# Optimization experiments

Hardware: AMD Instinct MI355X
Metric: run time of the kernel (lower is better)

The kernel has to match this reference:

```python
import jax, jax.numpy as jnp
import numpy as np
import math

BS, N, D_MODEL, H = 8, 1024, 512, 8
D_K = D_MODEL // H


def setup_inputs() -> dict:
    key = jax.random.key(0)
    ks = jax.random.split(key, 12)
    s = 1.0 / math.sqrt(D_MODEL)
    inp = {
        "query": jax.random.normal(ks[0], (BS, N, D_MODEL), jnp.float32),
        "key": jax.random.normal(ks[1], (BS, N, D_MODEL), jnp.float32),
        "value": jax.random.normal(ks[2], (BS, N, D_MODEL), jnp.float32),
        "wc_matrix": jax.random.normal(ks[3], (BS, N, N), jnp.float32),
        "Wq": jax.random.normal(ks[4], (D_MODEL, D_MODEL), jnp.float32) * s,
        "bq": jnp.zeros((D_MODEL,), jnp.float32),
        "Wk": jax.random.normal(ks[5], (D_MODEL, D_MODEL), jnp.float32) * s,
        "bk": jnp.zeros((D_MODEL,), jnp.float32),
        "Wv": jax.random.normal(ks[6], (D_MODEL, D_MODEL), jnp.float32) * s,
        "bv": jnp.zeros((D_MODEL,), jnp.float32),
        "Wo": jax.random.normal(ks[7], (D_MODEL, D_MODEL), jnp.float32) * s,
        "bo": jnp.zeros((D_MODEL,), jnp.float32),
    }
    return inp


def _split_heads(x):
    # (bs, N, d_model) -> (bs, h, N, d_k)
    b, n, _ = x.shape
    return x.reshape(b, n, H, D_K).transpose(0, 2, 1, 3)


def reference(query, key, value, wc_matrix, Wq, bq, Wk, bk, Wv, bv, Wo, bo):
    # Linear projections (torch Linear: x @ W.T + b), split into heads
    q = _split_heads(query @ Wq.T + bq)
    k = _split_heads(key @ Wk.T + bk)
    v = _split_heads(value @ Wv.T + bv)

    # scores: (bs, h, N, N)
    scores = jnp.einsum("bhnd,bhmd->bhnm", q, k) / jnp.sqrt(jnp.float32(D_K))
    # WC modulation: scores * softmax(wc)[:, None] + scores  (softmax_wc=True, residual=True)
    wc_sm = jax.nn.softmax(wc_matrix, axis=-1)[:, None]  # (bs, 1, N, N)
    scores = scores * wc_sm + scores
    p_attn = jax.nn.softmax(scores, axis=-1)  # dropout is identity in eval

    a = jnp.einsum("bhnm,bhmd->bhnd", p_attn, v)
    a = a.transpose(0, 2, 1, 3).reshape(query.shape[0], -1, D_MODEL)
    return a @ Wo.T + bo
```

## Files before the change

### kernel.cpp

```cpp
#include <hip/hip_runtime.h>
#include <math.h>


#define BS 8
#define SEQ 1024
#define DM 512
#define NH 8
#define DK 64
#define ROWS (BS * SEQ)

typedef __bf16 bf16_t;
typedef bf16_t bf16x8 __attribute__((ext_vector_type(8)));
typedef bf16_t bf16x4 __attribute__((ext_vector_type(4)));
typedef float f32x4 __attribute__((ext_vector_type(4)));

__device__ inline f32x4 mfma32(bf16x8 a, bf16x8 b, f32x4 c) {
  return __builtin_amdgcn_mfma_f32_16x16x32_bf16(a, b, c, 0, 0, 0);
}

__device__ inline void gload_lds16(const bf16_t* g, bf16_t* l) {
  __builtin_amdgcn_global_load_lds(
      (const __attribute__((address_space(1))) void*)g,
      (__attribute__((address_space(3))) void*)l, 16, 0, 0);
}

__global__ __launch_bounds__(256) void cvt_kernel(
    const float* q, const float* k, const float* v,
    const float* wq, const float* wk, const float* wv, const float* wo,
    bf16_t* xq, bf16_t* xk, bf16_t* xv,
    bf16_t* wqb, bf16_t* wkb, bf16_t* wvb, bf16_t* wob) {
  const float* srcs[7] = {q, k, v, wq, wk, wv, wo};
  bf16_t* dsts[7] = {xq, xk, xv, wqb, wkb, wvb, wob};
  int b = blockIdx.x;
  int seg, boff;
  if (b < 1536) { seg = b >> 9; boff = b & 511; }
  else { seg = 3 + ((b - 1536) >> 5); boff = (b - 1536) & 31; }
  const float* src = srcs[seg] + (size_t)boff * 8192;
  bf16_t* dst = dsts[seg] + (size_t)boff * 8192;
  int t = threadIdx.x;
#pragma unroll
  for (int f = 0; f < 8; ++f) {
    int idx = (f * 256 + t) * 4;
    float4 x = *(const float4*)(src + idx);
    bf16x4 o;
    o[0] = (bf16_t)x.x; o[1] = (bf16_t)x.y; o[2] = (bf16_t)x.z; o[3] = (bf16_t)x.w;
    *(bf16x4*)(dst + idx) = o;
  }
}

__global__ __launch_bounds__(256) void wc_softmax_kernel(const float* __restrict__ wc,
                                                         bf16_t* __restrict__ G) {
  int row = blockIdx.x;
  const float* x = wc + (size_t)row * SEQ;
  bf16_t* y = G + (size_t)row * SEQ;
  int t = threadIdx.x;
  float4 v = *(const float4*)(x + t * 4);
  float m = fmaxf(fmaxf(v.x, v.y), fmaxf(v.z, v.w));
#pragma unroll
  for (int off = 32; off > 0; off >>= 1) m = fmaxf(m, __shfl_xor(m, off, 64));
  __shared__ float sm[4], ss[4];
  int w = t >> 6;
  if ((t & 63) == 0) sm[w] = m;
  __syncthreads();
  m = fmaxf(fmaxf(sm[0], sm[1]), fmaxf(sm[2], sm[3]));
  float4 e;
  e.x = __expf(v.x - m); e.y = __expf(v.y - m);
  e.z = __expf(v.z - m); e.w = __expf(v.w - m);
  float s = e.x + e.y + e.z + e.w;
#pragma unroll
  for (int off = 32; off > 0; off >>= 1) s += __shfl_xor(s, off, 64);
  if ((t & 63) == 0) ss[w] = s;
  __syncthreads();
  s = ss[0] + ss[1] + ss[2] + ss[3];
  float inv = 1.0f / s;
  bf16x4 g;
  g[0] = (bf16_t)(1.0f + e.x * inv);
  g[1] = (bf16_t)(1.0f + e.y * inv);
  g[2] = (bf16_t)(1.0f + e.z * inv);
  g[3] = (bf16_t)(1.0f + e.w * inv);
  *(bf16x4*)(y + t * 4) = g;
}

template <int BM, bool OUTF32>
__device__ inline void gemm_core(const bf16_t* X, const bf16_t* W,
                                 const float* bias, void* Cv,
                                 int mblk, int nblk) {
  __shared__ bf16_t As[2][BM * 32];
  __shared__ bf16_t Bs[2][128 * 32];
  int t = threadIdx.x, lane = t & 63, w = t >> 6;
  int quad = lane >> 4, l15 = lane & 15;
  constexpr int MT = BM / 32;
  int m0w = (w & 1) * (BM / 2), n0w = (w >> 1) * 64;
  int mbase = mblk * BM, nbase = nblk * 128;
  int lr = lane >> 2, l4 = lane & 3;
  f32x4 acc[MT][4] = {};

#pragma unroll
  for (int f = 0; f < BM / 64; ++f) {
    int i = f * 4 + w;
    gload_lds16(X + (size_t)(mbase + i * 16 + lr) * DM + l4 * 8, &As[0][i * 512]);
  }
#pragma unroll
  for (int f = 0; f < 2; ++f) {
    int i = f * 4 + w;
    gload_lds16(W + (size_t)(nbase + i * 16 + lr) * DM + l4 * 8, &Bs[0][i * 512]);
  }

  for (int it = 0; it < 16; ++it) {
    __syncthreads();
    int cb = it & 1;
    if (it + 1 < 16) {
      int kb = (it + 1) * 32, nb = (it + 1) & 1;
#pragma unroll
      for (int f = 0; f < BM / 64; ++f) {
        int i = f * 4 + w;
        gload_lds16(X + (size_t)(mbase + i * 16 + lr) * DM + kb + l4 * 8, &As[nb][i * 512]);
      }
#pragma unroll
      for (int f = 0; f < 2; ++f) {
        int i = f * 4 + w;
        gload_lds16(W + (size_t)(nbase + i * 16 + lr) * DM + kb + l4 * 8, &Bs[nb][i * 512]);
      }
    }
    bf16x8 af[MT], bfr[4];
#pragma unroll
    for (int mt = 0; mt < MT; ++mt)
      af[mt] = *(const bf16x8*)&As[cb][(m0w + mt * 16 + l15) * 32 + quad * 8];
#pragma unroll
    for (int nt = 0; nt < 4; ++nt)
      bfr[nt] = *(const bf16x8*)&Bs[cb][(n0w + nt * 16 + l15) * 32 + quad * 8];
#pragma unroll
    for (int mt = 0; mt < MT; ++mt)
#pragma unroll
      for (int nt = 0; nt < 4; ++nt)
        acc[mt][nt] = mfma32(af[mt], bfr[nt], acc[mt][nt]);
  }

#pragma unroll
  for (int nt = 0; nt < 4; ++nt) {
    int col = nbase + n0w + nt * 16 + l15;
    float bc = bias[col];
#pragma unroll
    for (int mt = 0; mt < MT; ++mt)
#pragma unroll
      for (int r = 0; r < 4; ++r) {
        int row = mbase + m0w + mt * 16 + quad * 4 + r;
        float vv = acc[mt][nt][r] + bc;
        if (OUTF32)
          ((float*)Cv)[(size_t)row * DM + col] = vv;
        else
          ((bf16_t*)Cv)[(size_t)row * DM + col] = (bf16_t)vv;
      }
  }
}

__global__ __launch_bounds__(256) void gemm_qkv_kernel(
    const bf16_t* xq, const bf16_t* xk, const bf16_t* xv,
    const bf16_t* wq, const bf16_t* wk, const bf16_t* wv,
    const float* bq, const float* bk, const float* bv,
    bf16_t* cq, bf16_t* ck, bf16_t* cv) {
  const bf16_t* Xarr[3] = {xq, xk, xv};
  const bf16_t* Warr[3] = {wq, wk, wv};
  const float* barr[3] = {bq, bk, bv};
  bf16_t* Carr[3] = {cq, ck, cv};
  int z = blockIdx.z;
  gemm_core<128, false>(Xarr[z], Warr[z], barr[z], Carr[z], blockIdx.x, blockIdx.y);
}

__global__ __launch_bounds__(256) void gemm_wo_kernel(const bf16_t* X, const bf16_t* W,
                                                      const float* bias, float* C) {
  gemm_core<64, true>(X, W, bias, C, blockIdx.x, blockIdx.y);
}

__global__ __launch_bounds__(256) void vtrans_kernel(const bf16_t* __restrict__ Vb,
                                                     bf16_t* __restrict__ Vt) {
  int mt = blockIdx.x;
  int bh = blockIdx.y;
  int b = bh >> 3, h = bh & 7;
  __shared__ bf16_t Ts[64][66];
  int t = threadIdx.x;
#pragma unroll
  for (int f = 0; f < 2; ++f) {
    int chunk = t + f * 256;
    int row = chunk >> 3;
    int c8 = (chunk & 7) * 8;
    bf16x8 v = *(const bf16x8*)&Vb[(size_t)(b * SEQ + mt * 64 + row) * DM + h * DK + c8];
#pragma unroll
    for (int j = 0; j < 8; ++j) Ts[c8 + j][row] = v[j];
  }
  __syncthreads();
#pragma unroll
  for (int f = 0; f < 2; ++f) {
    int chunk = t + f * 256;
    int d = chunk >> 3;
    int m8 = (chunk & 7) * 8;
    bf16x8 o;
#pragma unroll
    for (int j = 0; j < 8; ++j) o[j] = Ts[d][m8 + j];
    *(bf16x8*)&Vt[((size_t)(bh * DK + d)) * SEQ + mt * 64 + m8] = o;
  }
}

__global__ __launch_bounds__(256) void flash_mfma_kernel(const bf16_t* __restrict__ Qb,
                                                         const bf16_t* __restrict__ Kb,
                                                         const bf16_t* __restrict__ Vt,
                                                         const bf16_t* __restrict__ G,
                                                         bf16_t* __restrict__ Ab) {
  int qt = blockIdx.x, h = blockIdx.y, b = blockIdx.z;
  __shared__ bf16_t Qs[64][72];
  __shared__ bf16_t Ks[64][72];
  __shared__ bf16_t Vs[64][72];
  __shared__ bf16_t Ps[64][72];
  int t = threadIdx.x, lane = t & 63, w = t >> 6;
  int quad = lane >> 4, l15 = lane & 15;

#pragma unroll
  for (int f = 0; f < 2; ++f) {
    int chunk = t + f * 256;
    int row = chunk >> 3, k8 = (chunk & 7) * 8;
    *(bf16x8*)&Qs[row][k8] =
        *(const bf16x8*)&Qb[(size_t)(b * SEQ + qt * 64 + row) * DM + h * DK + k8];
  }
  __syncthreads();
  bf16x8 aq0 = *(const bf16x8*)&Qs[w * 16 + l15][quad * 8];
  bf16x8 aq1 = *(const bf16x8*)&Qs[w * 16 + l15][32 + quad * 8];

  float m_st = -INFINITY, l_st = 0.f;
  f32x4 o[4] = {};
  const size_t grow = (size_t)(b * SEQ + qt * 64 + w * 16 + l15) * SEQ;

  int srow[2], sk8[2];
#pragma unroll
  for (int f = 0; f < 2; ++f) {
    int chunk = t + f * 256;
    srow[f] = chunk >> 3;
    sk8[f] = (chunk & 7) * 8;
  }
  const bf16_t* Kbase = Kb + (size_t)b * SEQ * DM + h * DK;
  const bf16_t* Vbase = Vt + (size_t)(b * NH + h) * DK * SEQ;
  bf16x8 kreg[2], vreg[2];
  bf16x4 greg[4];
#pragma unroll
  for (int f = 0; f < 2; ++f) {
    kreg[f] = *(const bf16x8*)&Kbase[(size_t)srow[f] * DM + sk8[f]];
    vreg[f] = *(const bf16x8*)&Vbase[(size_t)srow[f] * SEQ + sk8[f]];
  }
#pragma unroll
  for (int ct = 0; ct < 4; ++ct)
    greg[ct] = *(const bf16x4*)&G[grow + ct * 16 + quad * 4];

  for (int mt = 0; mt < 16; ++mt) {
    __syncthreads();
#pragma unroll
    for (int f = 0; f < 2; ++f) {
      *(bf16x8*)&Ks[srow[f]][sk8[f]] = kreg[f];
      *(bf16x8*)&Vs[srow[f]][sk8[f]] = vreg[f];
    }
    __syncthreads();
    if (mt + 1 < 16) {
#pragma unroll
      for (int f = 0; f < 2; ++f) {
        kreg[f] = *(const bf16x8*)&Kbase[(size_t)((mt + 1) * 64 + srow[f]) * DM + sk8[f]];
        vreg[f] = *(const bf16x8*)&Vbase[(size_t)srow[f] * SEQ + (mt + 1) * 64 + sk8[f]];
      }
    }

    f32x4 s[4];
#pragma unroll
    for (int ct = 0; ct < 4; ++ct) {
      bf16x8 ak0 = *(const bf16x8*)&Ks[ct * 16 + l15][quad * 8];
      bf16x8 ak1 = *(const bf16x8*)&Ks[ct * 16 + l15][32 + quad * 8];
      f32x4 z = {};
      s[ct] = mfma32(ak1, aq1, mfma32(ak0, aq0, z));
    }

    float sv[4][4];
    float rm = -INFINITY;
#pragma unroll
    for (int ct = 0; ct < 4; ++ct) {
#pragma unroll
      for (int r = 0; r < 4; ++r) {
        float x = s[ct][r] * 0.125f * (float)greg[ct][r];
        sv[ct][r] = x;
        rm = fmaxf(rm, x);
      }
    }
    if (mt + 1 < 16) {
#pragma unroll
      for (int ct = 0; ct < 4; ++ct)
        greg[ct] = *(const bf16x4*)&G[grow + (mt + 1) * 64 + ct * 16 + quad * 4];
    }
    rm = fmaxf(rm, __shfl_xor(rm, 16, 64));
    rm = fmaxf(rm, __shfl_xor(rm, 32, 64));
    float mnew = fmaxf(m_st, rm);
    float alpha = __expf(m_st - mnew);
    m_st = mnew;

    float rs = 0.f;
#pragma unroll
    for (int ct = 0; ct < 4; ++ct) {
      bf16x4 pb;
#pragma unroll
      for (int r = 0; r < 4; ++r) {
        float p = __expf(sv[ct][r] - mnew);
        pb[r] = (bf16_t)p;
        rs += p;
      }
      *(bf16x4*)&Ps[w * 16 + l15][ct * 16 + quad * 4] = pb;
    }
    rs += __shfl_xor(rs, 16, 64);
    rs += __shfl_xor(rs, 32, 64);
    l_st = l_st * alpha + rs;

#pragma unroll
    for (int dt = 0; dt < 4; ++dt) {
      o[dt][0] *= alpha; o[dt][1] *= alpha; o[dt][2] *= alpha; o[dt][3] *= alpha;
    }
#pragma unroll
    for (int c = 0; c < 2; ++c) {
      bf16x8 bp = *(const bf16x8*)&Ps[w * 16 + l15][c * 32 + quad * 8];
#pragma unroll
      for (int dt = 0; dt < 4; ++dt) {
        bf16x8 av = *(const bf16x8*)&Vs[dt * 16 + l15][c * 32 + quad * 8];
        o[dt] = mfma32(av, bp, o[dt]);
      }
    }
  }

  float linv = 1.0f / l_st;
  size_t qrow = (size_t)(b * SEQ + qt * 64 + w * 16 + l15);
#pragma unroll
  for (int dt = 0; dt < 4; ++dt)
#pragma unroll
    for (int r = 0; r < 4; ++r)
      Ab[qrow * DM + h * DK + dt * 16 + quad * 4 + r] = (bf16_t)(o[dt][r] * linv);
}

extern "C" void kernel_launch(void* const* d_in, const int* in_sizes, int n_in,
                              void* d_out, int out_size, void* d_ws, size_t ws_size,
                              hipStream_t stream) {
  const float* query = (const float*)d_in[0];
  const float* key = (const float*)d_in[1];
  const float* value = (const float*)d_in[2];
  const float* wc = (const float*)d_in[3];
  const float* Wq = (const float*)d_in[4];
  const float* bq = (const float*)d_in[5];
  const float* Wk = (const float*)d_in[6];
  const float* bk = (const float*)d_in[7];
  const float* Wv = (const float*)d_in[8];
  const float* bv = (const float*)d_in[9];
  const float* Wo = (const float*)d_in[10];
  const float* bo = (const float*)d_in[11];
  float* out = (float*)d_out;

  const size_t ACT = (size_t)ROWS * DM;
  const size_t WSZ = (size_t)DM * DM;
  bf16_t* Qb = (bf16_t*)d_ws;
  bf16_t* Kb = Qb + ACT;
  bf16_t* Vb = Kb + ACT;
  bf16_t* Vt = Vb + ACT;
  bf16_t* Ab = Vt + ACT;
  bf16_t* G = Ab + ACT;
  bf16_t* Xq = G + (size_t)BS * SEQ * SEQ;
  bf16_t* Xk = Xq + ACT;
  bf16_t* Xv = Xk + ACT;
  bf16_t* Wqb = Xv + ACT;
  bf16_t* Wkb = Wqb + WSZ;
  bf16_t* Wvb = Wkb + WSZ;
  bf16_t* Wob = Wvb + WSZ;

  cvt_kernel<<<1664, 256, 0, stream>>>(query, key, value, Wq, Wk, Wv, Wo,
                                       Xq, Xk, Xv, Wqb, Wkb, Wvb, Wob);

  wc_softmax_kernel<<<BS * SEQ, 256, 0, stream>>>(wc, G);

  gemm_qkv_kernel<<<dim3(ROWS / 128, DM / 128, 3), 256, 0, stream>>>(
      Xq, Xk, Xv, Wqb, Wkb, Wvb, bq, bk, bv, Qb, Kb, Vb);

  vtrans_kernel<<<dim3(16, 64), 256, 0, stream>>>(Vb, Vt);

  flash_mfma_kernel<<<dim3(SEQ / 64, NH, BS), 256, 0, stream>>>(Qb, Kb, Vt, G, Ab);

  gemm_wo_kernel<<<dim3(ROWS / 64, DM / 128), 256, 0, stream>>>(Ab, Wob, bo, out);
}
```

Measured before the change: 230.0 us.

## Fuse prep kernels, write V transposed from GEMM, double-buffer 128-row flash tiles

Merges the fp32-to-bf16 conversion and the wc softmax into one prep launch, with one wave per softmax row instead of one block. The V projection epilogue now writes the per-head transposed layout directly, so the separate transpose kernel and its buffer go away. The flash kernel handles 128 query rows per block (two 16-row subtiles per wave) and double-buffers K/V in LDS, which reuses each K/V tile across more queries and drops one barrier per iteration. In exchange it uses more LDS and registers, and launches half as many flash blocks (512), which may lower occupancy.

```diff
diff --git a/kernel.cpp b/kernel.cpp
--- a/kernel.cpp
+++ b/kernel.cpp
@@ -24,67 +24,72 @@
       (__attribute__((address_space(3))) void*)l, 16, 0, 0);
 }
 
-__global__ __launch_bounds__(256) void cvt_kernel(
+__global__ __launch_bounds__(256) void prep_kernel(
     const float* q, const float* k, const float* v,
     const float* wq, const float* wk, const float* wv, const float* wo,
+    const float* wc,
     bf16_t* xq, bf16_t* xk, bf16_t* xv,
-    bf16_t* wqb, bf16_t* wkb, bf16_t* wvb, bf16_t* wob) {
-  const float* srcs[7] = {q, k, v, wq, wk, wv, wo};
-  bf16_t* dsts[7] = {xq, xk, xv, wqb, wkb, wvb, wob};
-  int b = blockIdx.x;
-  int seg, boff;
-  if (b < 1536) { seg = b >> 9; boff = b & 511; }
-  else { seg = 3 + ((b - 1536) >> 5); boff = (b - 1536) & 31; }
-  const float* src = srcs[seg] + (size_t)boff * 8192;
-  bf16_t* dst = dsts[seg] + (size_t)boff * 8192;
+    bf16_t* wqb, bf16_t* wkb, bf16_t* wvb, bf16_t* wob,
+    bf16_t* G) {
+  int blk = blockIdx.x;
   int t = threadIdx.x;
-#pragma unroll
-  for (int f = 0; f < 8; ++f) {
-    int idx = (f * 256 + t) * 4;
-    float4 x = *(const float4*)(src + idx);
-    bf16x4 o;
-    o[0] = (bf16_t)x.x; o[1] = (bf16_t)x.y; o[2] = (bf16_t)x.z; o[3] = (bf16_t)x.w;
-    *(bf16x4*)(dst + idx) = o;
-  }
-}
-
-__global__ __launch_bounds__(256) void wc_softmax_kernel(const float* __restrict__ wc,
-                                                         bf16_t* __restrict__ G) {
-  int row = blockIdx.x;
-  const float* x = wc + (size_t)row * SEQ;
-  bf16_t* y = G + (size_t)row * SEQ;
-  int t = threadIdx.x;
-  float4 v = *(const float4*)(x + t * 4);
-  float m = fmaxf(fmaxf(v.x, v.y), fmaxf(v.z, v.w));
-#pragma unroll
-  for (int off = 32; off > 0; off >>= 1) m = fmaxf(m, __shfl_xor(m, off, 64));
-  __shared__ float sm[4], ss[4];
-  int w = t >> 6;
-  if ((t & 63) == 0) sm[w] = m;
-  __syncthreads();
-  m = fmaxf(fmaxf(sm[0], sm[1]), fmaxf(sm[2], sm[3]));
-  float4 e;
-  e.x = __expf(v.x - m); e.y = __expf(v.y - m);
-  e.z = __expf(v.z - m); e.w = __expf(v.w - m);
-  float s = e.x + e.y + e.z + e.w;
-#pragma unroll
-  for (int off = 32; off > 0; off >>= 1) s += __shfl_xor(s, off, 64);
-  if ((t & 63) == 0) ss[w] = s;
-  __syncthreads();
-  s = ss[0] + ss[1] + ss[2] + ss[3];
-  float inv = 1.0f / s;
-  bf16x4 g;
-  g[0] = (bf16_t)(1.0f + e.x * inv);
-  g[1] = (bf16_t)(1.0f + e.y * inv);
-  g[2] = (bf16_t)(1.0f + e.z * inv);
-  g[3] = (bf16_t)(1.0f + e.w * inv);
-  *(bf16x4*)(y + t * 4) = g;
+  if (blk < 1664) {
+    const float* srcs[7] = {q, k, v, wq, wk, wv, wo};
+    bf16_t* dsts[7] = {xq, xk, xv, wqb, wkb, wvb, wob};
+    int seg, boff;
+    if (blk < 1536) { seg = blk >> 9; boff = blk & 511; }
+    else { seg = 3 + ((blk - 1536) >> 5); boff = (blk - 1536) & 31; }
+    const float* src = srcs[seg] + (size_t)boff * 8192;
+    bf16_t* dst = dsts[seg] + (size_t)boff * 8192;
+#pragma unroll
+    for (int f = 0; f < 8; ++f) {
+      int idx = (f * 256 + t) * 4;
+      float4 x = *(const float4*)(src + idx);
+      bf16x4 o;
+      o[0] = (bf16_t)x.x; o[1] = (bf16_t)x.y; o[2] = (bf16_t)x.z; o[3] = (bf16_t)x.w;
+      *(bf16x4*)(dst + idx) = o;
+    }
+  } else {
+    int row = (blk - 1664) * 4 + (t >> 6);
+    int l = t & 63;
+    const float* x = wc + (size_t)row * SEQ;
+    bf16_t* y = G + (size_t)row * SEQ;
+    float4 vv[4];
+#pragma unroll
+    for (int j = 0; j < 4; ++j) vv[j] = *(const float4*)(x + l * 4 + j * 256);
+    float m = -INFINITY;
+#pragma unroll
+    for (int j = 0; j < 4; ++j)
+      m = fmaxf(m, fmaxf(fmaxf(vv[j].x, vv[j].y), fmaxf(vv[j].z, vv[j].w)));
+#pragma unroll
+    for (int off = 1; off < 64; off <<= 1) m = fmaxf(m, __shfl_xor(m, off, 64));
+    float4 e[4];
+    float s = 0.f;
+#pragma unroll
+    for (int j = 0; j < 4; ++j) {
+      e[j].x = __expf(vv[j].x - m); e[j].y = __expf(vv[j].y - m);
+      e[j].z = __expf(vv[j].z - m); e[j].w = __expf(vv[j].w - m);
+      s += e[j].x + e[j].y + e[j].z + e[j].w;
+    }
+#pragma unroll
+    for (int off = 1; off < 64; off <<= 1) s += __shfl_xor(s, off, 64);
+    float inv = 1.0f / s;
+#pragma unroll
+    for (int j = 0; j < 4; ++j) {
+      bf16x4 g;
+      g[0] = (bf16_t)(1.0f + e[j].x * inv);
+      g[1] = (bf16_t)(1.0f + e[j].y * inv);
+      g[2] = (bf16_t)(1.0f + e[j].z * inv);
+      g[3] = (bf16_t)(1.0f + e[j].w * inv);
+      *(bf16x4*)(y + l * 4 + j * 256) = g;
+    }
+  }
 }
 
 template <int BM, bool OUTF32>
 __device__ inline void gemm_core(const bf16_t* X, const bf16_t* W,
                                  const float* bias, void* Cv,
-                                 int mblk, int nblk) {
+                                 int mblk, int nblk, bool vt_out) {
   __shared__ bf16_t As[2][BM * 32];
   __shared__ bf16_t Bs[2][128 * 32];
   int t = threadIdx.x, lane = t & 63, w = t >> 6;
@@ -136,21 +141,38 @@
         acc[mt][nt] = mfma32(af[mt], bfr[nt], acc[mt][nt]);
   }
 
-#pragma unroll
-  for (int nt = 0; nt < 4; ++nt) {
-    int col = nbase + n0w + nt * 16 + l15;
-    float bc = bias[col];
-#pragma unroll
-    for (int mt = 0; mt < MT; ++mt)
-#pragma unroll
-      for (int r = 0; r < 4; ++r) {
-        int row = mbase + m0w + mt * 16 + quad * 4 + r;
-        float vv = acc[mt][nt][r] + bc;
-        if (OUTF32)
-          ((float*)Cv)[(size_t)row * DM + col] = vv;
-        else
-          ((bf16_t*)Cv)[(size_t)row * DM + col] = (bf16_t)vv;
-      }
+  if (vt_out) {
+#pragma unroll
+    for (int nt = 0; nt < 4; ++nt) {
+      int col = nbase + n0w + nt * 16 + l15;
+      float bc = bias[col];
+#pragma unroll
+      for (int mt = 0; mt < MT; ++mt) {
+        int row = mbase + m0w + mt * 16 + quad * 4;
+        int bb = row >> 10, ml = row & 1023;
+        bf16x4 vv;
+#pragma unroll
+        for (int r = 0; r < 4; ++r) vv[r] = (bf16_t)(acc[mt][nt][r] + bc);
+        *(bf16x4*)&((bf16_t*)Cv)[((size_t)((bb * NH + (col >> 6)) * DK + (col & 63))) * SEQ + ml] = vv;
+      }
+    }
+  } else {
+#pragma unroll
+    for (int nt = 0; nt < 4; ++nt) {
+      int col = nbase + n0w + nt * 16 + l15;
+      float bc = bias[col];
+#pragma unroll
+      for (int mt = 0; mt < MT; ++mt)
+#pragma unroll
+        for (int r = 0; r < 4; ++r) {
+          int row = mbase + m0w + mt * 16 + quad * 4 + r;
+          float vv = acc[mt][nt][r] + bc;
+          if (OUTF32)
+            ((float*)Cv)[(size_t)row * DM + col] = vv;
+          else
+            ((bf16_t*)Cv)[(size_t)row * DM + col] = (bf16_t)vv;
+        }
+    }
   }
 }
 
@@ -158,47 +180,19 @@
     const bf16_t* xq, const bf16_t* xk, const bf16_t* xv,
     const bf16_t* wq, const bf16_t* wk, const bf16_t* wv,
     const float* bq, const float* bk, const float* bv,
-    bf16_t* cq, bf16_t* ck, bf16_t* cv) {
+    bf16_t* cq, bf16_t* ck, bf16_t* vt) {
   const bf16_t* Xarr[3] = {xq, xk, xv};
   const bf16_t* Warr[3] = {wq, wk, wv};
   const float* barr[3] = {bq, bk, bv};
-  bf16_t* Carr[3] = {cq, ck, cv};
+  bf16_t* Carr[3] = {cq, ck, vt};
   int z = blockIdx.z;
-  gemm_core<128, false>(Xarr[z], Warr[z], barr[z], Carr[z], blockIdx.x, blockIdx.y);
+  gemm_core<128, false>(Xarr[z], Warr[z], barr[z], Carr[z],
+                        blockIdx.x, blockIdx.y, z == 2);
 }
 
 __global__ __launch_bounds__(256) void gemm_wo_kernel(const bf16_t* X, const bf16_t* W,
                                                       const float* bias, float* C) {
-  gemm_core<64, true>(X, W, bias, C, blockIdx.x, blockIdx.y);
-}
-
-__global__ __launch_bounds__(256) void vtrans_kernel(const bf16_t* __restrict__ Vb,
-                                                     bf16_t* __restrict__ Vt) {
-  int mt = blockIdx.x;
-  int bh = blockIdx.y;
-  int b = bh >> 3, h = bh & 7;
-  __shared__ bf16_t Ts[64][66];
-  int t = threadIdx.x;
-#pragma unroll
-  for (int f = 0; f < 2; ++f) {
-    int chunk = t + f * 256;
-    int row = chunk >> 3;
-    int c8 = (chunk & 7) * 8;
-    bf16x8 v = *(const bf16x8*)&Vb[(size_t)(b * SEQ + mt * 64 + row) * DM + h * DK + c8];
-#pragma unroll
-    for (int j = 0; j < 8; ++j) Ts[c8 + j][row] = v[j];
-  }
-  __syncthreads();
-#pragma unroll
-  for (int f = 0; f < 2; ++f) {
-    int chunk = t + f * 256;
-    int d = chunk >> 3;
-    int m8 = (chunk & 7) * 8;
-    bf16x8 o;
-#pragma unroll
-    for (int j = 0; j < 8; ++j) o[j] = Ts[d][m8 + j];
-    *(bf16x8*)&Vt[((size_t)(bh * DK + d)) * SEQ + mt * 64 + m8] = o;
-  }
+  gemm_core<64, true>(X, W, bias, C, blockIdx.x, blockIdx.y, false);
 }
 
 __global__ __launch_bounds__(256) void flash_mfma_kernel(const bf16_t* __restrict__ Qb,
@@ -207,27 +201,20 @@
                                                          const bf16_t* __restrict__ G,
                                                          bf16_t* __restrict__ Ab) {
   int qt = blockIdx.x, h = blockIdx.y, b = blockIdx.z;
-  __shared__ bf16_t Qs[64][72];
-  __shared__ bf16_t Ks[64][72];
-  __shared__ bf16_t Vs[64][72];
-  __shared__ bf16_t Ps[64][72];
+  __shared__ bf16_t Qs[128][72];
+  __shared__ bf16_t Ks[2][64][72];
+  __shared__ bf16_t Vs[2][64][72];
+  __shared__ bf16_t Ps[128][72];
   int t = threadIdx.x, lane = t & 63, w = t >> 6;
   int quad = lane >> 4, l15 = lane & 15;
 
 #pragma unroll
-  for (int f = 0; f < 2; ++f) {
+  for (int f = 0; f < 4; ++f) {
     int chunk = t + f * 256;
     int row = chunk >> 3, k8 = (chunk & 7) * 8;
     *(bf16x8*)&Qs[row][k8] =
-        *(const bf16x8*)&Qb[(size_t)(b * SEQ + qt * 64 + row) * DM + h * DK + k8];
-  }
-  __syncthreads();
-  bf16x8 aq0 = *(const bf16x8*)&Qs[w * 16 + l15][quad * 8];
-  bf16x8 aq1 = *(const bf16x8*)&Qs[w * 16 + l15][32 + quad * 8];
-
-  float m_st = -INFINITY, l_st = 0.f;
-  f32x4 o[4] = {};
-  const size_t grow = (size_t)(b * SEQ + qt * 64 + w * 16 + l15) * SEQ;
+        *(const bf16x8*)&Qb[(size_t)(b * SEQ + qt * 128 + row) * DM + h * DK + k8];
+  }
 
   int srow[2], sk8[2];
 #pragma unroll
@@ -239,101 +226,146 @@
   const bf16_t* Kbase = Kb + (size_t)b * SEQ * DM + h * DK;
   const bf16_t* Vbase = Vt + (size_t)(b * NH + h) * DK * SEQ;
   bf16x8 kreg[2], vreg[2];
-  bf16x4 greg[4];
 #pragma unroll
   for (int f = 0; f < 2; ++f) {
     kreg[f] = *(const bf16x8*)&Kbase[(size_t)srow[f] * DM + sk8[f]];
     vreg[f] = *(const bf16x8*)&Vbase[(size_t)srow[f] * SEQ + sk8[f]];
   }
 #pragma unroll
-  for (int ct = 0; ct < 4; ++ct)
-    greg[ct] = *(const bf16x4*)&G[grow + ct * 16 + quad * 4];
+  for (int f = 0; f < 2; ++f) {
+    *(bf16x8*)&Ks[0][srow[f]][sk8[f]] = kreg[f];
+    *(bf16x8*)&Vs[0][srow[f]][sk8[f]] = vreg[f];
+  }
+#pragma unroll
+  for (int f = 0; f < 2; ++f) {
+    kreg[f] = *(const bf16x8*)&Kbase[(size_t)(64 + srow[f]) * DM + sk8[f]];
+    vreg[f] = *(const bf16x8*)&Vbase[(size_t)srow[f] * SEQ + 64 + sk8[f]];
+  }
+
+  size_t grow[2];
+  bf16x4 greg[2][4];
+#pragma unroll
+  for (int sub = 0; sub < 2; ++sub) {
+    grow[sub] = (size_t)(b * SEQ + qt * 128 + w * 32 + sub * 16 + l15) * SEQ;
+#pragma unroll
+    for (int ct = 0; ct < 4; ++ct)
+      greg[sub][ct] = *(const bf16x4*)&G[grow[sub] + ct * 16 + quad * 4];
+  }
+
+  __syncthreads();
+  bf16x8 aq[2][2];
+#pragma unroll
+  for (int sub = 0; sub < 2; ++sub) {
+    int qr = w * 32 + sub * 16 + l15;
+    aq[sub][0] = *(const bf16x8*)&Qs[qr][quad * 8];
+    aq[sub][1] = *(const bf16x8*)&Qs[qr][32 + quad * 8];
+  }
+
+  float m_st[2] = {-INFINITY, -INFINITY}, l_st[2] = {0.f, 0.f};
+  f32x4 o[2][4] = {};
 
   for (int mt = 0; mt < 16; ++mt) {
     __syncthreads();
-#pragma unroll
-    for (int f = 0; f < 2; ++f) {
-      *(bf16x8*)&Ks[srow[f]][sk8[f]] = kreg[f];
-      *(bf16x8*)&Vs[srow[f]][sk8[f]] = vreg[f];
-    }
-    __syncthreads();
+    int cb = mt & 1;
     if (mt + 1 < 16) {
+      int nb = (mt + 1) & 1;
 #pragma unroll
       for (int f = 0; f < 2; ++f) {
-        kreg[f] = *(const bf16x8*)&Kbase[(size_t)((mt + 1) * 64 + srow[f]) * DM + sk8[f]];
-        vreg[f] = *(const bf16x8*)&Vbase[(size_t)srow[f] * SEQ + (mt + 1) * 64 + sk8[f]];
-      }
-    }
-
-    f32x4 s[4];
+        *(bf16x8*)&Ks[nb][srow[f]][sk8[f]] = kreg[f];
+        *(bf16x8*)&Vs[nb][srow[f]][sk8[f]] = vreg[f];
+      }
+      if (mt + 2 < 16) {
+#pragma unroll
+        for (int f = 0; f < 2; ++f) {
+          kreg[f] = *(const bf16x8*)&Kbase[(size_t)((mt + 2) * 64 + srow[f]) * DM + sk8[f]];
+          vreg[f] = *(const bf16x8*)&Vbase[(size_t)srow[f] * SEQ + (mt + 2) * 64 + sk8[f]];
+        }
+      }
+    }
+
+    bf16x8 ak[4][2], av[4][2];
 #pragma unroll
     for (int ct = 0; ct < 4; ++ct) {
-      bf16x8 ak0 = *(const bf16x8*)&Ks[ct * 16 + l15][quad * 8];
-      bf16x8 ak1 = *(const bf16x8*)&Ks[ct * 16 + l15][32 + quad * 8];
-      f32x4 z = {};
-      s[ct] = mfma32(ak1, aq1, mfma32(ak0, aq0, z));
-    }
-
-    float sv[4][4];
-    float rm = -INFINITY;
-#pragma unroll
-    for (int ct = 0; ct < 4; ++ct) {
-#pragma unroll
-      for (int r = 0; r < 4; ++r) {
-        float x = s[ct][r] * 0.125f * (float)greg[ct][r];
-        sv[ct][r] = x;
-        rm = fmaxf(rm, x);
-      }
-    }
-    if (mt + 1 < 16) {
-#pragma unroll
-      for (int ct = 0; ct < 4; ++ct)
-        greg[ct] = *(const bf16x4*)&G[grow + (mt + 1) * 64 + ct * 16 + quad * 4];
-    }
-    rm = fmaxf(rm, __shfl_xor(rm, 16, 64));
-    rm = fmaxf(rm, __shfl_xor(rm, 32, 64));
-    float mnew = fmaxf(m_st, rm);
-    float alpha = __expf(m_st - mnew);
-    m_st = mnew;
-
-    float rs = 0.f;
-#pragma unroll
-    for (int ct = 0; ct < 4; ++ct) {
-      bf16x4 pb;
-#pragma unroll
-      for (int r = 0; r < 4; ++r) {
-        float p = __expf(sv[ct][r] - mnew);
-        pb[r] = (bf16_t)p;
-        rs += p;
-      }
-      *(bf16x4*)&Ps[w * 16 + l15][ct * 16 + quad * 4] = pb;
-    }
-    rs += __shfl_xor(rs, 16, 64);
-    rs += __shfl_xor(rs, 32, 64);
-    l_st = l_st * alpha + rs;
-
+      ak[ct][0] = *(const bf16x8*)&Ks[cb][ct * 16 + l15][quad * 8];
+      ak[ct][1] = *(const bf16x8*)&Ks[cb][ct * 16 + l15][32 + quad * 8];
+    }
 #pragma unroll
     for (int dt = 0; dt < 4; ++dt) {
-      o[dt][0] *= alpha; o[dt][1] *= alpha; o[dt][2] *= alpha; o[dt][3] *= alpha;
-    }
-#pragma unroll
-    for (int c = 0; c < 2; ++c) {
-      bf16x8 bp = *(const bf16x8*)&Ps[w * 16 + l15][c * 32 + quad * 8];
+      av[dt][0] = *(const bf16x8*)&Vs[cb][dt * 16 + l15][quad * 8];
+      av[dt][1] = *(const bf16x8*)&Vs[cb][dt * 16 + l15][32 + quad * 8];
+    }
+
+#pragma unroll
+    for (int sub = 0; sub < 2; ++sub) {
+      f32x4 s[4];
+#pragma unroll
+      for (int ct = 0; ct < 4; ++ct) {
+        f32x4 z = {};
+        s[ct] = mfma32(ak[ct][1], aq[sub][1], mfma32(ak[ct][0], aq[sub][0], z));
+      }
+      float sv[4][4];
+      float rm = -INFINITY;
+#pragma unroll
+      for (int ct = 0; ct < 4; ++ct) {
+#pragma unroll
+        for (int r = 0; r < 4; ++r) {
+          float x = s[ct][r] * 0.125f * (float)greg[sub][ct][r];
+          sv[ct][r] = x;
+          rm = fmaxf(rm, x);
+        }
+      }
+      if (mt + 1 < 16) {
+#pragma unroll
+        for (int ct = 0; ct < 4; ++ct)
+          greg[sub][ct] = *(const bf16x4*)&G[grow[sub] + (mt + 1) * 64 + ct * 16 + quad * 4];
+      }
+      rm = fmaxf(rm, __shfl_xor(rm, 16, 64));
+      rm = fmaxf(rm, __shfl_xor(rm, 32, 64));
+      float mnew = fmaxf(m_st[sub], rm);
+      float alpha = __expf(m_st[sub] - mnew);
+      m_st[sub] = mnew;
+
+      float rs = 0.f;
+#pragma unroll
+      for (int ct = 0; ct < 4; ++ct) {
+        bf16x4 pb;
+#pragma unroll
+        for (int r = 0; r < 4; ++r) {
+          float p = __expf(sv[ct][r] - mnew);
+          pb[r] = (bf16_t)p;
+          rs += p;
+        }
+        *(bf16x4*)&Ps[w * 32 + sub * 16 + l15][ct * 16 + quad * 4] = pb;
+      }
+      rs += __shfl_xor(rs, 16, 64);
+      rs += __shfl_xor(rs, 32, 64);
+      l_st[sub] = l_st[sub] * alpha + rs;
+
 #pragma unroll
       for (int dt = 0; dt < 4; ++dt) {
-        bf16x8 av = *(const bf16x8*)&Vs[dt * 16 + l15][c * 32 + quad * 8];
-        o[dt] = mfma32(av, bp, o[dt]);
-      }
-    }
-  }
-
-  float linv = 1.0f / l_st;
-  size_t qrow = (size_t)(b * SEQ + qt * 64 + w * 16 + l15);
-#pragma unroll
-  for (int dt = 0; dt < 4; ++dt)
-#pragma unroll
-    for (int r = 0; r < 4; ++r)
-      Ab[qrow * DM + h * DK + dt * 16 + quad * 4 + r] = (bf16_t)(o[dt][r] * linv);
+        o[sub][dt][0] *= alpha; o[sub][dt][1] *= alpha;
+        o[sub][dt][2] *= alpha; o[sub][dt][3] *= alpha;
+      }
+#pragma unroll
+      for (int c = 0; c < 2; ++c) {
+        bf16x8 bp = *(const bf16x8*)&Ps[w * 32 + sub * 16 + l15][c * 32 + quad * 8];
+#pragma unroll
+        for (int dt = 0; dt < 4; ++dt)
+          o[sub][dt] = mfma32(av[dt][c], bp, o[sub][dt]);
+      }
+    }
+  }
+
+#pragma unroll
+  for (int sub = 0; sub < 2; ++sub) {
+    float linv = 1.0f / l_st[sub];
+    size_t qrow = (size_t)(b * SEQ + qt * 128 + w * 32 + sub * 16 + l15);
+#pragma unroll
+    for (int dt = 0; dt < 4; ++dt)
+#pragma unroll
+      for (int r = 0; r < 4; ++r)
+        Ab[qrow * DM + h * DK + dt * 16 + quad * 4 + r] = (bf16_t)(o[sub][dt][r] * linv);
+  }
 }
 
 extern "C" void kernel_launch(void* const* d_in, const int* in_sizes, int n_in,
@@ -357,8 +389,7 @@
   const size_t WSZ = (size_t)DM * DM;
   bf16_t* Qb = (bf16_t*)d_ws;
   bf16_t* Kb = Qb + ACT;
-  bf16_t* Vb = Kb + ACT;
-  bf16_t* Vt = Vb + ACT;
+  bf16_t* Vt = Kb + ACT;
   bf16_t* Ab = Vt + ACT;
   bf16_t* G = Ab + ACT;
   bf16_t* Xq = G + (size_t)BS * SEQ * SEQ;
@@ -369,17 +400,13 @@
   bf16_t* Wvb = Wkb + WSZ;
   bf16_t* Wob = Wvb + WSZ;
 
-  cvt_kernel<<<1664, 256, 0, stream>>>(query, key, value, Wq, Wk, Wv, Wo,
-                                       Xq, Xk, Xv, Wqb, Wkb, Wvb, Wob);
-
-  wc_softmax_kernel<<<BS * SEQ, 256, 0, stream>>>(wc, G);
+  prep_kernel<<<3712, 256, 0, stream>>>(query, key, value, Wq, Wk, Wv, Wo, wc,
+                                        Xq, Xk, Xv, Wqb, Wkb, Wvb, Wob, G);
 
   gemm_qkv_kernel<<<dim3(ROWS / 128, DM / 128, 3), 256, 0, stream>>>(
-      Xq, Xk, Xv, Wqb, Wkb, Wvb, bq, bk, bv, Qb, Kb, Vb);
-
-  vtrans_kernel<<<dim3(16, 64), 256, 0, stream>>>(Vb, Vt);
-
-  flash_mfma_kernel<<<dim3(SEQ / 64, NH, BS), 256, 0, stream>>>(Qb, Kb, Vt, G, Ab);
+      Xq, Xk, Xv, Wqb, Wkb, Wvb, bq, bk, bv, Qb, Kb, Vt);
+
+  flash_mfma_kernel<<<dim3(SEQ / 128, NH, BS), 256, 0, stream>>>(Qb, Kb, Vt, G, Ab);
 
   gemm_wo_kernel<<<dim3(ROWS / 64, DM / 128), 256, 0, stream>>>(Ab, Wob, bo, out);
 }
```

Measured after the change: 232.4 us. No clear change (+1.1%).

## Fuse wc softmax into convert kernel, transpose V in GEMM epilogue, fold scale

Applied to the files above, without the earlier changes.

Merges the input/weight conversion kernel and the wc-softmax kernel into one launch. The softmax now uses one wavefront per row, writes fp32 G, and pre-multiplies G by 1/sqrt(dk)·log2(e). The QKV GEMM writes V directly in transposed per-head layout through an LDS epilogue, which removes the separate transpose kernel and its extra round trip. The flash kernel uses exp2 on the prescaled scores, saving a multiply per element. The cost is that G becomes fp32, which doubles its storage and the bandwidth the attention kernel spends reading it.

```diff
diff --git a/kernel.cpp b/kernel.cpp
--- a/kernel.cpp
+++ b/kernel.cpp
@@ -14,6 +14,8 @@
 typedef bf16_t bf16x4 __attribute__((ext_vector_type(4)));
 typedef float f32x4 __attribute__((ext_vector_type(4)));
 
+#define GSCALE 0.18033688011112043f
+
 __device__ inline f32x4 mfma32(bf16x8 a, bf16x8 b, f32x4 c) {
   return __builtin_amdgcn_mfma_f32_16x16x32_bf16(a, b, c, 0, 0, 0);
 }
@@ -24,69 +26,78 @@
       (__attribute__((address_space(3))) void*)l, 16, 0, 0);
 }
 
-__global__ __launch_bounds__(256) void cvt_kernel(
+__global__ __launch_bounds__(256) void prep_kernel(
     const float* q, const float* k, const float* v,
     const float* wq, const float* wk, const float* wv, const float* wo,
+    const float* wc,
     bf16_t* xq, bf16_t* xk, bf16_t* xv,
-    bf16_t* wqb, bf16_t* wkb, bf16_t* wvb, bf16_t* wob) {
-  const float* srcs[7] = {q, k, v, wq, wk, wv, wo};
-  bf16_t* dsts[7] = {xq, xk, xv, wqb, wkb, wvb, wob};
-  int b = blockIdx.x;
-  int seg, boff;
-  if (b < 1536) { seg = b >> 9; boff = b & 511; }
-  else { seg = 3 + ((b - 1536) >> 5); boff = (b - 1536) & 31; }
-  const float* src = srcs[seg] + (size_t)boff * 8192;
-  bf16_t* dst = dsts[seg] + (size_t)boff * 8192;
+    bf16_t* wqb, bf16_t* wkb, bf16_t* wvb, bf16_t* wob,
+    float* G) {
+  int blk = blockIdx.x;
   int t = threadIdx.x;
-#pragma unroll
-  for (int f = 0; f < 8; ++f) {
-    int idx = (f * 256 + t) * 4;
-    float4 x = *(const float4*)(src + idx);
-    bf16x4 o;
-    o[0] = (bf16_t)x.x; o[1] = (bf16_t)x.y; o[2] = (bf16_t)x.z; o[3] = (bf16_t)x.w;
-    *(bf16x4*)(dst + idx) = o;
-  }
-}
-
-__global__ __launch_bounds__(256) void wc_softmax_kernel(const float* __restrict__ wc,
-                                                         bf16_t* __restrict__ G) {
-  int row = blockIdx.x;
-  const float* x = wc + (size_t)row * SEQ;
-  bf16_t* y = G + (size_t)row * SEQ;
-  int t = threadIdx.x;
-  float4 v = *(const float4*)(x + t * 4);
-  float m = fmaxf(fmaxf(v.x, v.y), fmaxf(v.z, v.w));
-#pragma unroll
-  for (int off = 32; off > 0; off >>= 1) m = fmaxf(m, __shfl_xor(m, off, 64));
-  __shared__ float sm[4], ss[4];
-  int w = t >> 6;
-  if ((t & 63) == 0) sm[w] = m;
-  __syncthreads();
-  m = fmaxf(fmaxf(sm[0], sm[1]), fmaxf(sm[2], sm[3]));
-  float4 e;
-  e.x = __expf(v.x - m); e.y = __expf(v.y - m);
-  e.z = __expf(v.z - m); e.w = __expf(v.w - m);
-  float s = e.x + e.y + e.z + e.w;
-#pragma unroll
-  for (int off = 32; off > 0; off >>= 1) s += __shfl_xor(s, off, 64);
-  if ((t & 63) == 0) ss[w] = s;
-  __syncthreads();
-  s = ss[0] + ss[1] + ss[2] + ss[3];
-  float inv = 1.0f / s;
-  bf16x4 g;
-  g[0] = (bf16_t)(1.0f + e.x * inv);
-  g[1] = (bf16_t)(1.0f + e.y * inv);
-  g[2] = (bf16_t)(1.0f + e.z * inv);
-  g[3] = (bf16_t)(1.0f + e.w * inv);
-  *(bf16x4*)(y + t * 4) = g;
+  if (blk < 1664) {
+    const float* src;
+    bf16_t* dst;
+    if (blk < 512)       { src = q  + (size_t)blk * 8192;          dst = xq  + (size_t)blk * 8192; }
+    else if (blk < 1024) { src = k  + (size_t)(blk - 512) * 8192;  dst = xk  + (size_t)(blk - 512) * 8192; }
+    else if (blk < 1536) { src = v  + (size_t)(blk - 1024) * 8192; dst = xv  + (size_t)(blk - 1024) * 8192; }
+    else if (blk < 1568) { src = wq + (size_t)(blk - 1536) * 8192; dst = wqb + (size_t)(blk - 1536) * 8192; }
+    else if (blk < 1600) { src = wk + (size_t)(blk - 1568) * 8192; dst = wkb + (size_t)(blk - 1568) * 8192; }
+    else if (blk < 1632) { src = wv + (size_t)(blk - 1600) * 8192; dst = wvb + (size_t)(blk - 1600) * 8192; }
+    else                 { src = wo + (size_t)(blk - 1632) * 8192; dst = wob + (size_t)(blk - 1632) * 8192; }
+#pragma unroll
+    for (int f = 0; f < 8; ++f) {
+      int idx = (f * 256 + t) * 4;
+      float4 x = *(const float4*)(src + idx);
+      bf16x4 o;
+      o[0] = (bf16_t)x.x; o[1] = (bf16_t)x.y; o[2] = (bf16_t)x.z; o[3] = (bf16_t)x.w;
+      *(bf16x4*)(dst + idx) = o;
+    }
+  } else {
+    int row = (blk - 1664) * 4 + (t >> 6);
+    int l = t & 63;
+    const float* x = wc + (size_t)row * SEQ;
+    float* y = G + (size_t)row * SEQ;
+    float4 vv[4];
+#pragma unroll
+    for (int j = 0; j < 4; ++j) vv[j] = *(const float4*)(x + l * 4 + j * 256);
+    float m = -INFINITY;
+#pragma unroll
+    for (int j = 0; j < 4; ++j)
+      m = fmaxf(m, fmaxf(fmaxf(vv[j].x, vv[j].y), fmaxf(vv[j].z, vv[j].w)));
+#pragma unroll
+    for (int off = 1; off < 64; off <<= 1) m = fmaxf(m, __shfl_xor(m, off, 64));
+    float4 e[4];
+    float s = 0.f;
+#pragma unroll
+    for (int j = 0; j < 4; ++j) {
+      e[j].x = __expf(vv[j].x - m); e[j].y = __expf(vv[j].y - m);
+      e[j].z = __expf(vv[j].z - m); e[j].w = __expf(vv[j].w - m);
+      s += e[j].x + e[j].y + e[j].z + e[j].w;
+    }
+#pragma unroll
+    for (int off = 1; off < 64; off <<= 1) s += __shfl_xor(s, off, 64);
+    float inv = 1.0f / s;
+#pragma unroll
+    for (int j = 0; j < 4; ++j) {
+      float4 g;
+      g.x = (1.0f + e[j].x * inv) * GSCALE;
+      g.y = (1.0f + e[j].y * inv) * GSCALE;
+      g.z = (1.0f + e[j].z * inv) * GSCALE;
+      g.w = (1.0f + e[j].w * inv) * GSCALE;
+      *(float4*)(y + l * 4 + j * 256) = g;
+    }
+  }
 }
 
 template <int BM, bool OUTF32>
 __device__ inline void gemm_core(const bf16_t* X, const bf16_t* W,
                                  const float* bias, void* Cv,
-                                 int mblk, int nblk) {
-  __shared__ bf16_t As[2][BM * 32];
-  __shared__ bf16_t Bs[2][128 * 32];
+                                 int mblk, int nblk, bool vt_out) {
+  constexpr int SMEM_ELTS = (BM == 128) ? 16640 : (2 * BM * 32 + 2 * 128 * 32);
+  __shared__ bf16_t smem[SMEM_ELTS];
+  bf16_t* As = smem;
+  bf16_t* Bs = smem + 2 * BM * 32;
   int t = threadIdx.x, lane = t & 63, w = t >> 6;
   int quad = lane >> 4, l15 = lane & 15;
   constexpr int MT = BM / 32;
@@ -98,12 +109,12 @@
 #pragma unroll
   for (int f = 0; f < BM / 64; ++f) {
     int i = f * 4 + w;
-    gload_lds16(X + (size_t)(mbase + i * 16 + lr) * DM + l4 * 8, &As[0][i * 512]);
+    gload_lds16(X + (size_t)(mbase + i * 16 + lr) * DM + l4 * 8, &As[i * 512]);
   }
 #pragma unroll
   for (int f = 0; f < 2; ++f) {
     int i = f * 4 + w;
-    gload_lds16(W + (size_t)(nbase + i * 16 + lr) * DM + l4 * 8, &Bs[0][i * 512]);
+    gload_lds16(W + (size_t)(nbase + i * 16 + lr) * DM + l4 * 8, &Bs[i * 512]);
   }
 
   for (int it = 0; it < 16; ++it) {
@@ -114,21 +125,23 @@
 #pragma unroll
       for (int f = 0; f < BM / 64; ++f) {
         int i = f * 4 + w;
-        gload_lds16(X + (size_t)(mbase + i * 16 + lr) * DM + kb + l4 * 8, &As[nb][i * 512]);
+        gload_lds16(X + (size_t)(mbase + i * 16 + lr) * DM + kb + l4 * 8,
+                    &As[nb * BM * 32 + i * 512]);
       }
 #pragma unroll
       for (int f = 0; f < 2; ++f) {
         int i = f * 4 + w;
-        gload_lds16(W + (size_t)(nbase + i * 16 + lr) * DM + kb + l4 * 8, &Bs[nb][i * 512]);
+        gload_lds16(W + (size_t)(nbase + i * 16 + lr) * DM + kb + l4 * 8,
+                    &Bs[nb * 128 * 32 + i * 512]);
       }
     }
     bf16x8 af[MT], bfr[4];
 #pragma unroll
     for (int mt = 0; mt < MT; ++mt)
-      af[mt] = *(const bf16x8*)&As[cb][(m0w + mt * 16 + l15) * 32 + quad * 8];
+      af[mt] = *(const bf16x8*)&As[cb * BM * 32 + (m0w + mt * 16 + l15) * 32 + quad * 8];
 #pragma unroll
     for (int nt = 0; nt < 4; ++nt)
-      bfr[nt] = *(const bf16x8*)&Bs[cb][(n0w + nt * 16 + l15) * 32 + quad * 8];
+      bfr[nt] = *(const bf16x8*)&Bs[cb * 128 * 32 + (n0w + nt * 16 + l15) * 32 + quad * 8];
 #pragma unroll
     for (int mt = 0; mt < MT; ++mt)
 #pragma unroll
@@ -136,21 +149,49 @@
         acc[mt][nt] = mfma32(af[mt], bfr[nt], acc[mt][nt]);
   }
 
-#pragma unroll
-  for (int nt = 0; nt < 4; ++nt) {
-    int col = nbase + n0w + nt * 16 + l15;
-    float bc = bias[col];
-#pragma unroll
-    for (int mt = 0; mt < MT; ++mt)
-#pragma unroll
-      for (int r = 0; r < 4; ++r) {
-        int row = mbase + m0w + mt * 16 + quad * 4 + r;
-        float vv = acc[mt][nt][r] + bc;
-        if (OUTF32)
-          ((float*)Cv)[(size_t)row * DM + col] = vv;
-        else
-          ((bf16_t*)Cv)[(size_t)row * DM + col] = (bf16_t)vv;
-      }
+  if (vt_out) {
+    bf16_t* Cs = smem;
+    __syncthreads();
+#pragma unroll
+    for (int nt = 0; nt < 4; ++nt) {
+      int col = n0w + nt * 16 + l15;
+      float bc = bias[nbase + col];
+#pragma unroll
+      for (int mt = 0; mt < MT; ++mt) {
+        int ml = m0w + mt * 16 + quad * 4;
+        bf16x4 vv;
+#pragma unroll
+        for (int r = 0; r < 4; ++r) vv[r] = (bf16_t)(acc[mt][nt][r] + bc);
+        *(bf16x4*)&Cs[col * 130 + ml] = vv;
+      }
+    }
+    __syncthreads();
+    int bb = mbase >> 10, ml0 = mbase & 1023;
+#pragma unroll
+    for (int f = 0; f < 8; ++f) {
+      int chunk = t + f * 256;
+      int col = chunk >> 4, m8 = (chunk & 15) * 8;
+      bf16x8 val = *(const bf16x8*)&Cs[col * 130 + m8];
+      int d = (nbase + col) & 63, hh = (nbase + col) >> 6;
+      *(bf16x8*)&((bf16_t*)Cv)[((size_t)((bb * NH + hh) * DK + d)) * SEQ + ml0 + m8] = val;
+    }
+  } else {
+#pragma unroll
+    for (int nt = 0; nt < 4; ++nt) {
+      int col = nbase + n0w + nt * 16 + l15;
+      float bc = bias[col];
+#pragma unroll
+      for (int mt = 0; mt < MT; ++mt)
+#pragma unroll
+        for (int r = 0; r < 4; ++r) {
+          int row = mbase + m0w + mt * 16 + quad * 4 + r;
+          float vv = acc[mt][nt][r] + bc;
+          if (OUTF32)
+            ((float*)Cv)[(size_t)row * DM + col] = vv;
+          else
+            ((bf16_t*)Cv)[(size_t)row * DM + col] = (bf16_t)vv;
+        }
+    }
   }
 }
 
@@ -158,53 +199,27 @@
     const bf16_t* xq, const bf16_t* xk, const bf16_t* xv,
     const bf16_t* wq, const bf16_t* wk, const bf16_t* wv,
     const float* bq, const float* bk, const float* bv,
-    bf16_t* cq, bf16_t* ck, bf16_t* cv) {
-  const bf16_t* Xarr[3] = {xq, xk, xv};
-  const bf16_t* Warr[3] = {wq, wk, wv};
-  const float* barr[3] = {bq, bk, bv};
-  bf16_t* Carr[3] = {cq, ck, cv};
+    bf16_t* cq, bf16_t* ck, bf16_t* vt) {
   int z = blockIdx.z;
-  gemm_core<128, false>(Xarr[z], Warr[z], barr[z], Carr[z], blockIdx.x, blockIdx.y);
+  const bf16_t* X;
+  const bf16_t* W;
+  const float* bias;
+  bf16_t* C;
+  if (z == 0)      { X = xq; W = wq; bias = bq; C = cq; }
+  else if (z == 1) { X = xk; W = wk; bias = bk; C = ck; }
+  else             { X = xv; W = wv; bias = bv; C = vt; }
+  gemm_core<128, false>(X, W, bias, C, blockIdx.x, blockIdx.y, z == 2);
 }
 
 __global__ __launch_bounds__(256) void gemm_wo_kernel(const bf16_t* X, const bf16_t* W,
                                                       const float* bias, float* C) {
-  gemm_core<64, true>(X, W, bias, C, blockIdx.x, blockIdx.y);
-}
-
-__global__ __launch_bounds__(256) void vtrans_kernel(const bf16_t* __restrict__ Vb,
-                                                     bf16_t* __restrict__ Vt) {
-  int mt = blockIdx.x;
-  int bh = blockIdx.y;
-  int b = bh >> 3, h = bh & 7;
-  __shared__ bf16_t Ts[64][66];
-  int t = threadIdx.x;
-#pragma unroll
-  for (int f = 0; f < 2; ++f) {
-    int chunk = t + f * 256;
-    int row = chunk >> 3;
-    int c8 = (chunk & 7) * 8;
-    bf16x8 v = *(const bf16x8*)&Vb[(size_t)(b * SEQ + mt * 64 + row) * DM + h * DK + c8];
-#pragma unroll
-    for (int j = 0; j < 8; ++j) Ts[c8 + j][row] = v[j];
-  }
-  __syncthreads();
-#pragma unroll
-  for (int f = 0; f < 2; ++f) {
-    int chunk = t + f * 256;
-    int d = chunk >> 3;
-    int m8 = (chunk & 7) * 8;
-    bf16x8 o;
-#pragma unroll
-    for (int j = 0; j < 8; ++j) o[j] = Ts[d][m8 + j];
-    *(bf16x8*)&Vt[((size_t)(bh * DK + d)) * SEQ + mt * 64 + m8] = o;
-  }
+  gemm_core<64, true>(X, W, bias, C, blockIdx.x, blockIdx.y, false);
 }
 
 __global__ __launch_bounds__(256) void flash_mfma_kernel(const bf16_t* __restrict__ Qb,
                                                          const bf16_t* __restrict__ Kb,
                                                          const bf16_t* __restrict__ Vt,
-                                                         const bf16_t* __restrict__ G,
+                                                         const float* __restrict__ G,
                                                          bf16_t* __restrict__ Ab) {
   int qt = blockIdx.x, h = blockIdx.y, b = blockIdx.z;
   __shared__ bf16_t Qs[64][72];
@@ -239,7 +254,7 @@
   const bf16_t* Kbase = Kb + (size_t)b * SEQ * DM + h * DK;
   const bf16_t* Vbase = Vt + (size_t)(b * NH + h) * DK * SEQ;
   bf16x8 kreg[2], vreg[2];
-  bf16x4 greg[4];
+  f32x4 greg[4];
 #pragma unroll
   for (int f = 0; f < 2; ++f) {
     kreg[f] = *(const bf16x8*)&Kbase[(size_t)srow[f] * DM + sk8[f]];
@@ -247,7 +262,7 @@
   }
 #pragma unroll
   for (int ct = 0; ct < 4; ++ct)
-    greg[ct] = *(const bf16x4*)&G[grow + ct * 16 + quad * 4];
+    greg[ct] = *(const f32x4*)&G[grow + ct * 16 + quad * 4];
 
   for (int mt = 0; mt < 16; ++mt) {
     __syncthreads();
@@ -280,7 +295,7 @@
     for (int ct = 0; ct < 4; ++ct) {
 #pragma unroll
       for (int r = 0; r < 4; ++r) {
-        float x = s[ct][r] * 0.125f * (float)greg[ct][r];
+        float x = s[ct][r] * greg[ct][r];
         sv[ct][r] = x;
         rm = fmaxf(rm, x);
       }
@@ -288,12 +303,12 @@
     if (mt + 1 < 16) {
 #pragma unroll
       for (int ct = 0; ct < 4; ++ct)
-        greg[ct] = *(const bf16x4*)&G[grow + (mt + 1) * 64 + ct * 16 + quad * 4];
+        greg[ct] = *(const f32x4*)&G[grow + (mt + 1) * 64 + ct * 16 + quad * 4];
     }
     rm = fmaxf(rm, __shfl_xor(rm, 16, 64));
     rm = fmaxf(rm, __shfl_xor(rm, 32, 64));
     float mnew = fmaxf(m_st, rm);
-    float alpha = __expf(m_st - mnew);
+    float alpha = __builtin_amdgcn_exp2f(m_st - mnew);
     m_st = mnew;
 
     float rs = 0.f;
@@ -302,7 +317,7 @@
       bf16x4 pb;
 #pragma unroll
       for (int r = 0; r < 4; ++r) {
-        float p = __expf(sv[ct][r] - mnew);
+        float p = __builtin_amdgcn_exp2f(sv[ct][r] - mnew);
         pb[r] = (bf16_t)p;
         rs += p;
       }
@@ -357,27 +372,22 @@
   const size_t WSZ = (size_t)DM * DM;
   bf16_t* Qb = (bf16_t*)d_ws;
   bf16_t* Kb = Qb + ACT;
-  bf16_t* Vb = Kb + ACT;
-  bf16_t* Vt = Vb + ACT;
+  bf16_t* Vt = Kb + ACT;
   bf16_t* Ab = Vt + ACT;
-  bf16_t* G = Ab + ACT;
-  bf16_t* Xq = G + (size_t)BS * SEQ * SEQ;
+  bf16_t* Xq = Ab + ACT;
   bf16_t* Xk = Xq + ACT;
   bf16_t* Xv = Xk + ACT;
   bf16_t* Wqb = Xv + ACT;
   bf16_t* Wkb = Wqb + WSZ;
   bf16_t* Wvb = Wkb + WSZ;
   bf16_t* Wob = Wvb + WSZ;
-
-  cvt_kernel<<<1664, 256, 0, stream>>>(query, key, value, Wq, Wk, Wv, Wo,
-                                       Xq, Xk, Xv, Wqb, Wkb, Wvb, Wob);
-
-  wc_softmax_kernel<<<BS * SEQ, 256, 0, stream>>>(wc, G);
+  float* G = (float*)(Wob + WSZ);
+
+  prep_kernel<<<3712, 256, 0, stream>>>(query, key, value, Wq, Wk, Wv, Wo, wc,
+                                        Xq, Xk, Xv, Wqb, Wkb, Wvb, Wob, G);
 
   gemm_qkv_kernel<<<dim3(ROWS / 128, DM / 128, 3), 256, 0, stream>>>(
-      Xq, Xk, Xv, Wqb, Wkb, Wvb, bq, bk, bv, Qb, Kb, Vb);
-
-  vtrans_kernel<<<dim3(16, 64), 256, 0, stream>>>(Vb, Vt);
+      Xq, Xk, Xv, Wqb, Wkb, Wvb, bq, bk, bv, Qb, Kb, Vt);
 
   flash_mfma_kernel<<<dim3(SEQ / 64, NH, BS), 256, 0, stream>>>(Qb, Kb, Vt, G, Ab);
 
```

New measurement: 236.0 us. 1.03x slower.
